# Kernel optimization log

Hardware: AMD Instinct MI355X
Metric: run time of the kernel (lower is better)

Reference implementation:

```python
import jax, jax.numpy as jnp
import numpy as np

L, N, D_IN = 4, 2048, 1024
H, DH = 8, 64
INNER = H * DH          # 512
D_OUT = D_IN            # out_dim defaults to input_dim
SCALE = DH ** -0.5


def setup_inputs() -> dict:
    key = jax.random.key(0)
    ks = jax.random.split(key, 7)
    x = jax.random.normal(ks[0], (L, N, D_IN), jnp.float32)
    # torch Linear weights are [out_features, in_features]; xavier-ish scale
    Wq = jax.random.normal(ks[1], (INNER, D_IN), jnp.float32) * 0.03
    Wk = jax.random.normal(ks[2], (INNER, D_IN), jnp.float32) * 0.03
    Wv = jax.random.normal(ks[3], (INNER, D_IN), jnp.float32) * 0.03
    Wo = jax.random.normal(ks[4], (D_OUT, INNER), jnp.float32) * 0.03
    bo = jnp.zeros((D_OUT,), jnp.float32)
    # boolean key-padding mask [L, n]; ensure at least one valid key per row
    mask = jax.random.uniform(ks[5], (L, N)) < 0.9
    mask = mask.at[:, 0].set(True)
    return {"x": x, "Wq": Wq, "Wk": Wk, "Wv": Wv, "Wo": Wo, "bo": bo, "mask": mask}


def reference(x, Wq, Wk, Wv, Wo, bo, mask):
    # projections (Linear: y = x @ W^T), split heads: L n (h d) -> l h n d
    def split_heads(t):
        return t.reshape(L, N, H, DH).transpose(0, 2, 1, 3)

    q = split_heads(jnp.einsum('lnd,ed->lne', x, Wq))
    k = split_heads(jnp.einsum('lnd,ed->lne', x, Wk))  # context defaults to x
    v = split_heads(jnp.einsum('lnd,ed->lne', x, Wv))

    sim = jnp.einsum('lhnd,lhmd->lhnm', q, k) * SCALE   # [L,H,N,N]
    neg = -jnp.finfo(sim.dtype).max
    sim = jnp.where(mask[:, None, None, :], sim, neg)   # mask over key dim
    attn = jax.nn.softmax(sim, axis=-1)

    out = jnp.einsum('lhnm,lhmd->lhnd', attn, v)        # [L,H,N,DH]
    out = out.transpose(0, 2, 1, 3).reshape(L, N, INNER)
    return out @ Wo.T + bo                               # [L,N,D_OUT]
```

## Files before the change

kernel.cpp:

```cpp
#include <hip/hip_runtime.h>
#include <hip/hip_bf16.h>

#define L_DIM 4
#define N_DIM 2048
#define DIN   1024
#define H_DIM 8
#define DH    64
#define INNER 512

typedef __attribute__((ext_vector_type(8))) short short8;
typedef __attribute__((ext_vector_type(4))) float f32x4;

__device__ __forceinline__ unsigned short f2bf(float f) {
  unsigned u = __builtin_bit_cast(unsigned, f);
  u += 0x7fffu + ((u >> 16) & 1u);
  return (unsigned short)(u >> 16);
}

__device__ __forceinline__ unsigned cvtpk(float a, float b) {
  unsigned r;
  asm("v_cvt_pk_bf16_f32 %0, %1, %2" : "=v"(r) : "v"(a), "v"(b));
  return r;
}

__device__ __forceinline__ float fexp2(float x) {
  float r;
  asm("v_exp_f32 %0, %1" : "=v"(r) : "v"(x));
  return r;
}

typedef __attribute__((address_space(3))) unsigned int lds_uint;
typedef const __attribute__((address_space(1))) unsigned int glob_uint;
__device__ __forceinline__ void gl_lds16(const unsigned short* g,
                                         unsigned short* l) {
  __builtin_amdgcn_global_load_lds((glob_uint*)g, (lds_uint*)l, 16, 0, 0);
}

__global__ void cast_all(const float* __restrict__ x,
                         const float* __restrict__ wq,
                         const float* __restrict__ wk,
                         const float* __restrict__ wv,
                         const float* __restrict__ wo,
                         unsigned short* __restrict__ xb,
                         unsigned short* __restrict__ w3,
                         unsigned short* __restrict__ wob,
                         const unsigned char* __restrict__ mraw,
                         float* __restrict__ bias) {
  __shared__ int votes[2];
  int bid = blockIdx.x, t = threadIdx.x;
  if (bid == 10240) {
    if (t < 2) votes[t] = 0;
    __syncthreads();
    const unsigned int* m32 = (const unsigned int*)mraw;
    int anyf = 0, any8 = 0;
    for (int i = t; i < 2048; i += 256) {
      unsigned w = m32[i];
      if (w == 0x3f800000u) anyf = 1;
      if (w & 0xffffff00u) any8 = 1;
    }
    if (anyf) atomicOr(&votes[0], 1);
    if (any8) atomicOr(&votes[1], 1);
    __syncthreads();
    int fmt = votes[0] ? 2 : (votes[1] ? 1 : 0);
    for (int i = t; i < L_DIM * N_DIM; i += 256) {
      int mv;
      if (fmt == 2)      mv = ((const float*)mraw)[i] != 0.0f;
      else if (fmt == 1) mv = mraw[i] != 0;
      else               mv = ((const int*)mraw)[i] != 0;
      bias[i] = mv ? 0.0f : -1e30f;
    }
    return;
  }
  int i = (bid * 256 + t) * 4;
  const float* src; unsigned short* dst; int off;
  if (i < 8388608)      { src = x;  dst = xb;           off = i; }
  else if (i < 8912896) { src = wq; dst = w3;           off = i - 8388608; }
  else if (i < 9437184) { src = wk; dst = w3 + 524288;  off = i - 8912896; }
  else if (i < 9961472) { src = wv; dst = w3 + 1048576; off = i - 9437184; }
  else                  { src = wo; dst = wob;          off = i - 9961472; }
  float4 f = *(const float4*)(src + off);
  ushort4 o4;
  o4.x = f2bf(f.x); o4.y = f2bf(f.y); o4.z = f2bf(f.z); o4.w = f2bf(f.w);
  *(ushort4*)(dst + off) = o4;
}

__launch_bounds__(256, 3)
__global__ void gemm_qkv(const unsigned short* __restrict__ xb,
                         const unsigned short* __restrict__ w3,
                         unsigned short* __restrict__ qp,
                         unsigned short* __restrict__ kp,
                         unsigned short* __restrict__ vtp) {
  __shared__ __align__(16) unsigned short Sh[8704];
  unsigned short* As = Sh;
  unsigned short* Bs = Sh + 4096;
  const int tid = threadIdx.x, lane = tid & 63, wid = tid >> 6;
  const int l16 = lane & 15, quad = lane >> 4;
  const int wm = wid >> 1, wn = wid & 1;
  const int m0 = blockIdx.x * 128, n0 = blockIdx.y * 128;

  f32x4 acc[4][4] = {};
  for (int kt = 0; kt < DIN; kt += 32) {
    __syncthreads();
#pragma unroll
    for (int it = 0; it < 2; ++it) {
      int c = it * 256 + wid * 64 + lane;
      int row = c >> 2, kseg = c & 3;
      unsigned short* lbase = &As[(it * 256 + wid * 64) * 8];
      gl_lds16(&xb[(m0 + row) * DIN + kt + kseg * 8], lbase);
      unsigned short* lbase2 = &Bs[(it * 256 + wid * 64) * 8];
      gl_lds16(&w3[(n0 + row) * DIN + kt + kseg * 8], lbase2);
    }
    __syncthreads();
    short8 af[4], bf[4];
#pragma unroll
    for (int mt = 0; mt < 4; ++mt)
      af[mt] = *(const short8*)&As[(wm * 64 + mt * 16 + l16) * 32 + quad * 8];
#pragma unroll
    for (int nt = 0; nt < 4; ++nt)
      bf[nt] = *(const short8*)&Bs[(wn * 64 + nt * 16 + l16) * 32 + quad * 8];
#pragma unroll
    for (int mt = 0; mt < 4; ++mt)
#pragma unroll
      for (int nt = 0; nt < 4; ++nt)
        acc[mt][nt] = __builtin_amdgcn_mfma_f32_16x16x32_bf16(
            af[mt], bf[nt], acc[mt][nt], 0, 0, 0);
  }
  if (blockIdx.y >= 8) {
    const int l = m0 >> 11, mloc = m0 & 2047;
#pragma unroll
    for (int chunk = 0; chunk < 2; ++chunk) {
      __syncthreads();
      if (wn == chunk) {
#pragma unroll
        for (int mt = 0; mt < 4; ++mt)
#pragma unroll
          for (int nt = 0; nt < 4; ++nt) {
            int col = nt * 16 + l16;
            int rowb = wm * 64 + mt * 16 + quad * 4;
            ushort4 pv;
            pv.x = f2bf(acc[mt][nt][0]);
            pv.y = f2bf(acc[mt][nt][1]);
            pv.z = f2bf(acc[mt][nt][2]);
            pv.w = f2bf(acc[mt][nt][3]);
            *(ushort4*)&Sh[col * 136 + rowb] = pv;
          }
      }
      __syncthreads();
      int hh = ((n0 + chunk * 64) & 511) >> 6;
#pragma unroll
      for (int it = 0; it < 4; ++it) {
        int c = it * 256 + tid;
        int cl = c >> 4, seg = c & 15;
        short8 vv = *(const short8*)&Sh[cl * 136 + seg * 8];
        *(short8*)&vtp[((size_t)((l * H_DIM + hh) * DH + cl)) * N_DIM + mloc +
                       seg * 8] = vv;
      }
    }
  } else {
#pragma unroll
    for (int mt = 0; mt < 4; ++mt)
#pragma unroll
      for (int nt = 0; nt < 4; ++nt)
#pragma unroll
        for (int r = 0; r < 4; ++r) {
          int grow = m0 + wm * 64 + mt * 16 + quad * 4 + r;
          int gcol = n0 + wn * 64 + nt * 16 + l16;
          unsigned short bv = f2bf(acc[mt][nt][r]);
          int h = (gcol & 511) >> 6, d = gcol & 63;
          int l = grow >> 11, n = grow & 2047;
          unsigned short* dst = (gcol >> 9) ? kp : qp;
          dst[(((l * H_DIM + h) * N_DIM + n) * DH) + d] = bv;
        }
  }
}

#define PW_S 64
__launch_bounds__(128, 2)
__global__ void attn_kernel(const unsigned short* __restrict__ qg,
                            const unsigned short* __restrict__ kg,
                            const unsigned short* __restrict__ vtg,
                            const float* __restrict__ bias,
                            unsigned short* __restrict__ aout) {
  __shared__ __align__(16) unsigned short Ks[2][64 * 64];
  __shared__ __align__(16) unsigned short Vs[2][64 * 64];
  __shared__ __align__(16) unsigned short Pw[64 * PW_S];
  const int tid = threadIdx.x, lane = tid & 63, wid = tid >> 6;
  const int l16 = lane & 15, quad = lane >> 4;
  const int bid = blockIdx.x;
  const int xcd = bid & 7, j = bid >> 3;
  const int lh = xcd * 4 + (j >> 5);
  const int q0 = (j & 31) << 6;
  const int l = lh >> 3, h = lh & 7;
  const unsigned short* Qb = qg + (size_t)lh * N_DIM * DH;
  const unsigned short* Kb = kg + (size_t)lh * N_DIM * DH;
  const unsigned short* Vt = vtg + (size_t)lh * DH * N_DIM;
  const float* bl = bias + l * N_DIM;

  short8 qf[2][2];
#pragma unroll
  for (int mt = 0; mt < 2; ++mt)
#pragma unroll
    for (int ks = 0; ks < 2; ++ks)
      qf[mt][ks] = *(const short8*)&Qb[(q0 + wid * 32 + mt * 16 + l16) * DH +
                                       ks * 32 + quad * 8];

  f32x4 o[2][4] = {};
  float lsum[2] = {0.f, 0.f};

  int kof[4], ldsb[4];
  size_t vof[4];
#pragma unroll
  for (int it = 0; it < 4; ++it) {
    int cb = it * 128 + wid * 64, c = cb + lane;
    int rr = c >> 3, sl = c & 7, gs = (sl + rr) & 7;
    kof[it] = rr * DH + gs * 8;
    vof[it] = (size_t)rr * N_DIM + gs * 8;
    ldsb[it] = cb * 8;
  }

#pragma unroll
  for (int it = 0; it < 4; ++it) {
    gl_lds16(&Kb[kof[it]], &Ks[0][ldsb[it]]);
    gl_lds16(&Vt[vof[it]], &Vs[0][ldsb[it]]);
  }

  for (int t = 0; t < 32; ++t) {
    const int kv = t << 6, buf = t & 1;
    __syncthreads();
    if (t < 31) {
      int kv2 = kv + 64, b2 = buf ^ 1;
#pragma unroll
      for (int it = 0; it < 4; ++it) {
        gl_lds16(&Kb[(kv2 << 6) + kof[it]], &Ks[b2][ldsb[it]]);
        gl_lds16(&Vt[vof[it] + kv2], &Vs[b2][ldsb[it]]);
      }
    }
    const unsigned short* Kst = Ks[buf];
    const unsigned short* Vst = Vs[buf];

    f32x4 sc[2][4] = {};
#pragma unroll
    for (int nt = 0; nt < 4; ++nt)
#pragma unroll
      for (int ks = 0; ks < 2; ++ks) {
        int s = (ks * 4 + quad - l16) & 7;
        short8 kf = *(const short8*)&Kst[(nt * 16 + l16) * 64 + s * 8];
#pragma unroll
        for (int mt = 0; mt < 2; ++mt)
          sc[mt][nt] = __builtin_amdgcn_mfma_f32_16x16x32_bf16(
              kf, qf[mt][ks], sc[mt][nt], 0, 0, 0);
      }
#pragma unroll
    for (int mt = 0; mt < 2; ++mt) {
      unsigned short* pr = &Pw[(wid * 32 + mt * 16 + l16) * PW_S];
#pragma unroll
      for (int nt = 0; nt < 4; ++nt) {
        float4 b4 = *(const float4*)&bl[kv + nt * 16 + quad * 4];
        float p0 = fexp2(fmaf(sc[mt][nt][0], 0.18033688011f, b4.x));
        float p1 = fexp2(fmaf(sc[mt][nt][1], 0.18033688011f, b4.y));
        float p2 = fexp2(fmaf(sc[mt][nt][2], 0.18033688011f, b4.z));
        float p3 = fexp2(fmaf(sc[mt][nt][3], 0.18033688011f, b4.w));
        lsum[mt] += (p0 + p1) + (p2 + p3);
        uint2 pk = make_uint2(cvtpk(p0, p1), cvtpk(p2, p3));
        int gk = nt * 2 + (quad >> 1);
        int s = (gk + l16) & 7;
        *(uint2*)&pr[s * 8 + (quad & 1) * 4] = pk;
      }
    }
#pragma unroll
    for (int g = 0; g < 2; ++g) {
      short8 pa[2];
#pragma unroll
      for (int mt = 0; mt < 2; ++mt) {
        int sp = (g * 4 + quad + l16) & 7;
        pa[mt] = *(const short8*)&Pw[(wid * 32 + mt * 16 + l16) * PW_S +
                                     sp * 8];
      }
#pragma unroll
      for (int nt = 0; nt < 4; ++nt) {
        int dd = nt * 16 + l16;
        int sv2 = (g * 4 + quad - l16) & 7;
        short8 vb = *(const short8*)&Vst[dd * 64 + sv2 * 8];
#pragma unroll
        for (int mt = 0; mt < 2; ++mt)
          o[mt][nt] = __builtin_amdgcn_mfma_f32_16x16x32_bf16(
              pa[mt], vb, o[mt][nt], 0, 0, 0);
      }
    }
  }
#pragma unroll
  for (int mt = 0; mt < 2; ++mt) {
    lsum[mt] += __shfl_xor(lsum[mt], 16);
    lsum[mt] += __shfl_xor(lsum[mt], 32);
  }
#pragma unroll
  for (int mt = 0; mt < 2; ++mt)
#pragma unroll
    for (int r = 0; r < 4; ++r) {
      float inv = 1.f / __shfl(lsum[mt], quad * 4 + r);
      int row = q0 + wid * 32 + mt * 16 + quad * 4 + r;
#pragma unroll
      for (int nt = 0; nt < 4; ++nt)
        aout[(size_t)(l * N_DIM + row) * INNER + h * DH + nt * 16 + l16] =
            f2bf(o[mt][nt][r] * inv);
    }
}

__launch_bounds__(256, 3)
__global__ void gemm_out(const unsigned short* __restrict__ a,
                         const unsigned short* __restrict__ wo,
                         const float* __restrict__ bo,
                         float* __restrict__ out) {
  __shared__ unsigned short As[128 * 32];
  __shared__ unsigned short Bs[128 * 32];
  const int tid = threadIdx.x, lane = tid & 63, wid = tid >> 6;
  const int l16 = lane & 15, quad = lane >> 4;
  const int wm = wid >> 1, wn = wid & 1;
  const int m0 = blockIdx.x * 128, n0 = blockIdx.y * 128;

  f32x4 acc[4][4] = {};
  for (int kt = 0; kt < INNER; kt += 32) {
    __syncthreads();
#pragma unroll
    for (int it = 0; it < 2; ++it) {
      int c = it * 256 + wid * 64 + lane;
      int row = c >> 2, kseg = c & 3;
      unsigned short* lbase = &As[(it * 256 + wid * 64) * 8];
      gl_lds16(&a[(m0 + row) * INNER + kt + kseg * 8], lbase);
      unsigned short* lbase2 = &Bs[(it * 256 + wid * 64) * 8];
      gl_lds16(&wo[(n0 + row) * INNER + kt + kseg * 8], lbase2);
    }
    __syncthreads();
    short8 af[4], bf[4];
#pragma unroll
    for (int mt = 0; mt < 4; ++mt)
      af[mt] = *(const short8*)&As[(wm * 64 + mt * 16 + l16) * 32 + quad * 8];
#pragma unroll
    for (int nt = 0; nt < 4; ++nt)
      bf[nt] = *(const short8*)&Bs[(wn * 64 + nt * 16 + l16) * 32 + quad * 8];
#pragma unroll
    for (int mt = 0; mt < 4; ++mt)
#pragma unroll
      for (int nt = 0; nt < 4; ++nt)
        acc[mt][nt] = __builtin_amdgcn_mfma_f32_16x16x32_bf16(
            af[mt], bf[nt], acc[mt][nt], 0, 0, 0);
  }
#pragma unroll
  for (int mt = 0; mt < 4; ++mt)
#pragma unroll
    for (int nt = 0; nt < 4; ++nt)
#pragma unroll
      for (int r = 0; r < 4; ++r) {
        int grow = m0 + wm * 64 + mt * 16 + quad * 4 + r;
        int gcol = n0 + wn * 64 + nt * 16 + l16;
        out[(size_t)grow * DIN + gcol] = acc[mt][nt][r] + bo[gcol];
      }
}

extern "C" void kernel_launch(void* const* d_in, const int* in_sizes, int n_in,
                              void* d_out, int out_size, void* d_ws,
                              size_t ws_size, hipStream_t stream) {
  const float* x  = (const float*)d_in[0];
  const float* Wq = (const float*)d_in[1];
  const float* Wk = (const float*)d_in[2];
  const float* Wv = (const float*)d_in[3];
  const float* Wo = (const float*)d_in[4];
  const float* bo = (const float*)d_in[5];
  const unsigned char* mask = (const unsigned char*)d_in[6];
  float* out = (float*)d_out;

  char* ws = (char*)d_ws;
  unsigned short* xb  = (unsigned short*)(ws + 0);
  unsigned short* w3  = (unsigned short*)(ws + 16777216);
  unsigned short* wob = (unsigned short*)(ws + 19922944);
  unsigned short* q   = (unsigned short*)(ws + 20971520);
  unsigned short* k   = (unsigned short*)(ws + 29360128);
  unsigned short* vt  = (unsigned short*)(ws + 37748736);
  unsigned short* att = (unsigned short*)(ws + 46137344);
  float* bias         = (float*)(ws + 54525952);

  cast_all<<<10241, 256, 0, stream>>>(x, Wq, Wk, Wv, Wo, xb, w3, wob, mask,
                                      bias);
  gemm_qkv<<<dim3(64, 12), 256, 0, stream>>>(xb, w3, q, k, vt);
  attn_kernel<<<1024, 128, 0, stream>>>(q, k, vt, bias, att);
  gemm_out<<<dim3(64, 8), 256, 0, stream>>>(att, wob, bo, out);
}
```

Before: 214.8 us.

## Double-buffer LDS tiles in QKV and output projection GEMMs

Both projection GEMMs now use two LDS buffers for their A and B tiles. The first tile is prefetched before the K-loop, and each iteration issues the global-to-LDS loads for the next K-slice before running MFMAs on the current one, so there is one barrier per iteration instead of two. Global address offsets are also precomputed once outside the loop. This is meant to hide global load latency behind matrix math. The cost is doubled LDS per block (32 KB), which could limit occupancy.

```diff
diff --git a/kernel.cpp b/kernel.cpp
--- a/kernel.cpp
+++ b/kernel.cpp
@@ -90,27 +90,42 @@
                          unsigned short* __restrict__ qp,
                          unsigned short* __restrict__ kp,
                          unsigned short* __restrict__ vtp) {
-  __shared__ __align__(16) unsigned short Sh[8704];
-  unsigned short* As = Sh;
-  unsigned short* Bs = Sh + 4096;
+  __shared__ __align__(16) unsigned short Sh[16384];
   const int tid = threadIdx.x, lane = tid & 63, wid = tid >> 6;
   const int l16 = lane & 15, quad = lane >> 4;
   const int wm = wid >> 1, wn = wid & 1;
   const int m0 = blockIdx.x * 128, n0 = blockIdx.y * 128;
 
+  int aoff[2], boff[2], lofs[2];
+#pragma unroll
+  for (int it = 0; it < 2; ++it) {
+    int c = it * 256 + wid * 64 + lane;
+    int row = c >> 2, kseg = c & 3;
+    aoff[it] = (m0 + row) * DIN + kseg * 8;
+    boff[it] = (n0 + row) * DIN + kseg * 8;
+    lofs[it] = (it * 256 + wid * 64) * 8;
+  }
+
+#pragma unroll
+  for (int it = 0; it < 2; ++it) {
+    gl_lds16(&xb[aoff[it]], &Sh[lofs[it]]);
+    gl_lds16(&w3[boff[it]], &Sh[8192 + lofs[it]]);
+  }
+
   f32x4 acc[4][4] = {};
-  for (int kt = 0; kt < DIN; kt += 32) {
+  for (int t = 0; t < 32; ++t) {
+    const int buf = t & 1;
     __syncthreads();
-#pragma unroll
-    for (int it = 0; it < 2; ++it) {
-      int c = it * 256 + wid * 64 + lane;
-      int row = c >> 2, kseg = c & 3;
-      unsigned short* lbase = &As[(it * 256 + wid * 64) * 8];
-      gl_lds16(&xb[(m0 + row) * DIN + kt + kseg * 8], lbase);
-      unsigned short* lbase2 = &Bs[(it * 256 + wid * 64) * 8];
-      gl_lds16(&w3[(n0 + row) * DIN + kt + kseg * 8], lbase2);
-    }
-    __syncthreads();
+    if (t < 31) {
+      int kt2 = (t + 1) * 32, b2 = buf ^ 1;
+#pragma unroll
+      for (int it = 0; it < 2; ++it) {
+        gl_lds16(&xb[aoff[it] + kt2], &Sh[b2 * 4096 + lofs[it]]);
+        gl_lds16(&w3[boff[it] + kt2], &Sh[8192 + b2 * 4096 + lofs[it]]);
+      }
+    }
+    const unsigned short* As = &Sh[buf * 4096];
+    const unsigned short* Bs = &Sh[8192 + buf * 4096];
     short8 af[4], bf[4];
 #pragma unroll
     for (int mt = 0; mt < 4; ++mt)
@@ -311,26 +326,42 @@
                          const unsigned short* __restrict__ wo,
                          const float* __restrict__ bo,
                          float* __restrict__ out) {
-  __shared__ unsigned short As[128 * 32];
-  __shared__ unsigned short Bs[128 * 32];
+  __shared__ __align__(16) unsigned short Sh[16384];
   const int tid = threadIdx.x, lane = tid & 63, wid = tid >> 6;
   const int l16 = lane & 15, quad = lane >> 4;
   const int wm = wid >> 1, wn = wid & 1;
   const int m0 = blockIdx.x * 128, n0 = blockIdx.y * 128;
 
+  int aoff[2], boff[2], lofs[2];
+#pragma unroll
+  for (int it = 0; it < 2; ++it) {
+    int c = it * 256 + wid * 64 + lane;
+    int row = c >> 2, kseg = c & 3;
+    aoff[it] = (m0 + row) * INNER + kseg * 8;
+    boff[it] = (n0 + row) * INNER + kseg * 8;
+    lofs[it] = (it * 256 + wid * 64) * 8;
+  }
+
+#pragma unroll
+  for (int it = 0; it < 2; ++it) {
+    gl_lds16(&a[aoff[it]], &Sh[lofs[it]]);
+    gl_lds16(&wo[boff[it]], &Sh[8192 + lofs[it]]);
+  }
+
   f32x4 acc[4][4] = {};
-  for (int kt = 0; kt < INNER; kt += 32) {
+  for (int t = 0; t < 16; ++t) {
+    const int buf = t & 1;
     __syncthreads();
-#pragma unroll
-    for (int it = 0; it < 2; ++it) {
-      int c = it * 256 + wid * 64 + lane;
-      int row = c >> 2, kseg = c & 3;
-      unsigned short* lbase = &As[(it * 256 + wid * 64) * 8];
-      gl_lds16(&a[(m0 + row) * INNER + kt + kseg * 8], lbase);
-      unsigned short* lbase2 = &Bs[(it * 256 + wid * 64) * 8];
-      gl_lds16(&wo[(n0 + row) * INNER + kt + kseg * 8], lbase2);
-    }
-    __syncthreads();
+    if (t < 15) {
+      int kt2 = (t + 1) * 32, b2 = buf ^ 1;
+#pragma unroll
+      for (int it = 0; it < 2; ++it) {
+        gl_lds16(&a[aoff[it] + kt2], &Sh[b2 * 4096 + lofs[it]]);
+        gl_lds16(&wo[boff[it] + kt2], &Sh[8192 + b2 * 4096 + lofs[it]]);
+      }
+    }
+    const unsigned short* As = &Sh[buf * 4096];
+    const unsigned short* Bs = &Sh[8192 + buf * 4096];
     short8 af[4], bf[4];
 #pragma unroll
     for (int mt = 0; mt < 4; ++mt)
```

New measurement: 215.1 us. No clear change (+0.2%).
